# Optimization experiments

Hardware: AMD Instinct MI355X
Metric: run time of the kernel (lower is better)

## Reference

```python
import jax, jax.numpy as jnp
import numpy as np


def _hadamard(n):
    # Sylvester construction; n must be a power of 2 (matches scipy.linalg.hadamard)
    H = np.array([[1.0]], dtype=np.float32)
    while H.shape[0] < n:
        H = np.block([[H, H], [H, -H]])
    return jnp.asarray(H)


def setup_inputs() -> dict:
    key = jax.random.key(0)
    k1, k2 = jax.random.split(key)
    shape = (524288, 3, 8, 8)  # [num_blocks, channels, 8, 8] SATD blocks
    return {
        "original": jax.random.normal(k1, shape, dtype=jnp.float32),
        "pred": jax.random.normal(k2, shape, dtype=jnp.float32),
    }


def reference(original, pred):
    n = original.shape[-1]  # last dim sizes the Hadamard matrix, as in the torch code
    H = _hadamard(n)  # [n, n]
    diff = original - pred  # [B, C, n, n]
    # torch.matmul(H, block): contract H columns with block rows (dim -2)
    t = jnp.einsum('ij,bcjw->bciw', H, diff)
    return jnp.sum(jnp.abs(t))
```

## Files before the change

kernel.cpp:

```cpp
#include <hip/hip_runtime.h>


typedef float fvec4 __attribute__((ext_vector_type(4)));

__device__ __forceinline__ float fwht_abssum(fvec4 t, int lane) {
    #pragma unroll
    for (int m = 2; m <= 8; m <<= 1) {
        const bool hi = (lane & m) != 0;
        fvec4 p;
        p.x = __shfl_xor(t.x, m, 64);
        p.y = __shfl_xor(t.y, m, 64);
        p.z = __shfl_xor(t.z, m, 64);
        p.w = __shfl_xor(t.w, m, 64);
        fvec4 add = t + p;
        fvec4 sub = p - t;
        t = hi ? sub : add;
    }
    return fabsf(t.x) + fabsf(t.y) + fabsf(t.z) + fabsf(t.w);
}

__global__ __launch_bounds__(256, 8) void satd_loss_kernel(
        const fvec4* __restrict__ orig, const fvec4* __restrict__ pred,
        float* __restrict__ out, int n4) {
    const int tid = blockIdx.x * blockDim.x + threadIdx.x;
    const int total = gridDim.x * blockDim.x;
    const int lane = threadIdx.x & 63;

    float acc = 0.0f;

    for (int i = tid; i < n4; i += 2 * total) {
        fvec4 a0 = orig[i];
        fvec4 b0 = pred[i];
        fvec4 a1 = orig[i + total];
        fvec4 b1 = pred[i + total];
        acc += fwht_abssum(a0 - b0, lane);
        acc += fwht_abssum(a1 - b1, lane);
    }

    #pragma unroll
    for (int off = 32; off > 0; off >>= 1)
        acc += __shfl_down(acc, off, 64);

    __shared__ float wsum[4];
    const int wid = threadIdx.x >> 6;
    if (lane == 0) wsum[wid] = acc;
    __syncthreads();

    if (threadIdx.x == 0) {
        float s = wsum[0] + wsum[1] + wsum[2] + wsum[3];
        atomicAdd(out, s);
    }
}

extern "C" void kernel_launch(void* const* d_in, const int* in_sizes, int n_in,
                              void* d_out, int out_size, void* d_ws, size_t ws_size,
                              hipStream_t stream) {
    const fvec4* orig = (const fvec4*)d_in[0];
    const fvec4* pred = (const fvec4*)d_in[1];
    float* out = (float*)d_out;

    const int nelem = in_sizes[0];
    const int n4 = nelem / 4;

    (void)hipMemsetAsync(out, 0, sizeof(float) * (size_t)out_size, stream);

    const int block = 256;
    const int grid = 8192;

    satd_loss_kernel<<<grid, block, 0, stream>>>(orig, pred, out, n4);
}
```

Before: 173.3 us.

## Stream inputs via async global-to-LDS loads with double-buffered chunk pipeline

Replaces the grid-stride direct loads with a per-block loop over fixed chunks. Each chunk's orig/pred tiles are fetched with global_load_lds into a double-buffered LDS array, and the next chunk is prefetched while the current one is transformed. Grid size and chunk counts are hardcoded to match the input size exactly, removing the bounds parameter. The aim is better latency hiding of the memory stream, at the cost of per-chunk barriers, fewer blocks, and no generality to other sizes.

```diff
diff --git a/kernel.cpp b/kernel.cpp
--- a/kernel.cpp
+++ b/kernel.cpp
@@ -2,6 +2,10 @@
 
 
 typedef float fvec4 __attribute__((ext_vector_type(4)));
+
+#define CHUNK_F4 512
+#define NCHUNKS 48
+#define GRID 1024
 
 __device__ __forceinline__ float fwht_abssum(fvec4 t, int lane) {
     #pragma unroll
@@ -19,34 +23,74 @@
     return fabsf(t.x) + fabsf(t.y) + fabsf(t.z) + fabsf(t.w);
 }
 
-__global__ __launch_bounds__(256, 8) void satd_loss_kernel(
+__global__ __launch_bounds__(256) void satd_loss_kernel(
         const fvec4* __restrict__ orig, const fvec4* __restrict__ pred,
-        float* __restrict__ out, int n4) {
-    const int tid = blockIdx.x * blockDim.x + threadIdx.x;
-    const int total = gridDim.x * blockDim.x;
-    const int lane = threadIdx.x & 63;
+        float* __restrict__ out) {
+    __shared__ fvec4 buf[2][2 * CHUNK_F4];
+    __shared__ float wsum[4];
+
+    const int t = threadIdx.x;
+    const int w = t >> 6;
+    const int lane = t & 63;
+    const int ch0 = blockIdx.x * NCHUNKS;
 
     float acc = 0.0f;
 
-    for (int i = tid; i < n4; i += 2 * total) {
-        fvec4 a0 = orig[i];
-        fvec4 b0 = pred[i];
-        fvec4 a1 = orig[i + total];
-        fvec4 b1 = pred[i + total];
-        acc += fwht_abssum(a0 - b0, lane);
-        acc += fwht_abssum(a1 - b1, lane);
+    auto stage = [&](int ch, int bs) {
+        const int cb = ch * CHUNK_F4;
+        #pragma unroll
+        for (int k = 0; k < 2; ++k) {
+            const int seg = 2 * w + k;
+            const fvec4* go = orig + cb + seg * 64 + lane;
+            const fvec4* gp = pred + cb + seg * 64 + lane;
+            __builtin_amdgcn_global_load_lds(
+                (const __attribute__((address_space(1))) void*)go,
+                (__attribute__((address_space(3))) void*)&buf[bs][seg * 64],
+                16, 0, 0);
+            __builtin_amdgcn_global_load_lds(
+                (const __attribute__((address_space(1))) void*)gp,
+                (__attribute__((address_space(3))) void*)&buf[bs][CHUNK_F4 + seg * 64],
+                16, 0, 0);
+        }
+    };
+
+    stage(ch0, 0);
+
+    for (int c = 0; c < NCHUNKS - 1; ++c) {
+        stage(ch0 + c + 1, (c + 1) & 1);
+        asm volatile("s_waitcnt vmcnt(4)" ::: "memory");
+        __builtin_amdgcn_s_barrier();
+        __builtin_amdgcn_sched_barrier(0);
+        {
+            const int bs = c & 1;
+            fvec4 d0 = buf[bs][t]       - buf[bs][CHUNK_F4 + t];
+            fvec4 d1 = buf[bs][t + 256] - buf[bs][CHUNK_F4 + t + 256];
+            acc += fwht_abssum(d0, lane);
+            acc += fwht_abssum(d1, lane);
+        }
+        __builtin_amdgcn_s_barrier();
+        __builtin_amdgcn_sched_barrier(0);
+    }
+
+    asm volatile("s_waitcnt vmcnt(0)" ::: "memory");
+    __builtin_amdgcn_s_barrier();
+    __builtin_amdgcn_sched_barrier(0);
+    {
+        const int bs = (NCHUNKS - 1) & 1;
+        fvec4 d0 = buf[bs][t]       - buf[bs][CHUNK_F4 + t];
+        fvec4 d1 = buf[bs][t + 256] - buf[bs][CHUNK_F4 + t + 256];
+        acc += fwht_abssum(d0, lane);
+        acc += fwht_abssum(d1, lane);
     }
 
     #pragma unroll
     for (int off = 32; off > 0; off >>= 1)
         acc += __shfl_down(acc, off, 64);
 
-    __shared__ float wsum[4];
-    const int wid = threadIdx.x >> 6;
-    if (lane == 0) wsum[wid] = acc;
+    if (lane == 0) wsum[w] = acc;
     __syncthreads();
 
-    if (threadIdx.x == 0) {
+    if (t == 0) {
         float s = wsum[0] + wsum[1] + wsum[2] + wsum[3];
         atomicAdd(out, s);
     }
@@ -59,13 +103,7 @@
     const fvec4* pred = (const fvec4*)d_in[1];
     float* out = (float*)d_out;
 
-    const int nelem = in_sizes[0];
-    const int n4 = nelem / 4;
-
     (void)hipMemsetAsync(out, 0, sizeof(float) * (size_t)out_size, stream);
 
-    const int block = 256;
-    const int grid = 8192;
-
-    satd_loss_kernel<<<grid, block, 0, stream>>>(orig, pred, out, n4);
+    satd_loss_kernel<<<GRID, 256, 0, stream>>>(orig, pred, out);
 }
```

After: 153.5 us. 1.13x faster.
